# Optimization experiments

Measured on AMD Instinct MI355X. Metric: run time of the kernel, lower is better.

The kernel has to match this reference:

```python
import jax, jax.numpy as jnp
import numpy as np

B, T, C, H = 8, 4096, 768, 64  # batch, seq, input_channels, head size


def setup_inputs() -> dict:
    key = jax.random.key(0)
    k1, k2, k3, k4 = jax.random.split(key, 4)
    scale = 1.0 / np.sqrt(C)
    return {
        "x": jax.random.normal(k1, (B, T, C), dtype=jnp.float32),
        "Wk": jax.random.normal(k2, (C, H), dtype=jnp.float32) * scale,
        "Wq": jax.random.normal(k3, (C, H), dtype=jnp.float32) * scale,
        "Wv": jax.random.normal(k4, (C, H), dtype=jnp.float32) * scale,
    }


def reference(x, Wk, Wq, Wv):
    Bc, Tc, Cc = x.shape
    k = x @ Wk  # [B,T,H]
    q = x @ Wq  # [B,T,H]
    v = x @ Wv  # [B,T,H]
    # Note: original scales by C**-0.5 where C = input_channels
    wei = jnp.einsum("bth,bTh->btT", q, k) * (Cc ** -0.5)
    causal = jnp.tril(jnp.ones((Tc, Tc), dtype=bool))
    wei = jnp.where(causal, wei, -jnp.inf)
    wei = jax.nn.softmax(wei, axis=-1)
    # dropout_prob = 0.0 -> identity
    out = jnp.einsum("btT,bTh->bth", wei, v)
    return out
```

## Files before the change

kernel.cpp:

```cpp
#include <hip/hip_runtime.h>

#define TT 4096
#define CCH 768
#define HH 64
#define BBA 8
#define MROWS (BBA*TT)
#define NCHUNK_PB 288

typedef __attribute__((ext_vector_type(8))) short short8;
typedef __attribute__((ext_vector_type(4))) float floatx4;
#if __has_builtin(__builtin_amdgcn_cvt_pk_bf16_f32)
typedef __attribute__((ext_vector_type(2))) __bf16 bf16x2;
#endif

__device__ inline ushort f2bf(float f) {
    union { float f; unsigned u; } v; v.f = f;
    unsigned r = v.u + 0x7fffu + ((v.u >> 16) & 1u);
    return (ushort)(r >> 16);
}

__device__ inline float bf2f(ushort h) {
    union { unsigned u; float f; } v; v.u = ((unsigned)h) << 16;
    return v.f;
}

__device__ inline unsigned pk_bf16(float a, float b) {
#if __has_builtin(__builtin_amdgcn_cvt_pk_bf16_f32)
    union { bf16x2 v; unsigned u; } cv;
    cv.v = __builtin_amdgcn_cvt_pk_bf16_f32(a, b);
    return cv.u;
#else
    union { float f; unsigned u; } x, y; x.f = a; y.f = b;
    unsigned ra = x.u + 0x7fffu + ((x.u >> 16) & 1u);
    unsigned rb = y.u + 0x7fffu + ((y.u >> 16) & 1u);
    return (ra >> 16) | (rb & 0xffff0000u);
#endif
}

__device__ inline float fast_exp2(float x) {
#if __has_builtin(__builtin_amdgcn_exp2f)
    return __builtin_amdgcn_exp2f(x);
#else
    return exp2f(x);
#endif
}

__global__ __launch_bounds__(256) void wt_kernel(const float* __restrict__ Wq,
                                                 const float* __restrict__ Wk,
                                                 const float* __restrict__ Wv,
                                                 ushort* __restrict__ wt) {
    __shared__ float tile[64][65];
    const int m = blockIdx.x / 12, kt = blockIdx.x % 12;
    const float* W = (m == 0) ? Wq : (m == 1) ? Wk : Wv;
    const int n = threadIdx.x & 63, r0 = threadIdx.x >> 6;
#pragma unroll
    for (int i = 0; i < 16; ++i) {
        int k = r0 * 16 + i;
        tile[k][n] = W[(kt * 64 + k) * 64 + n];
    }
    __syncthreads();
    const int k2 = threadIdx.x & 63, n2 = threadIdx.x >> 6;
#pragma unroll
    for (int i = 0; i < 16; ++i) {
        int nn = n2 * 16 + i;
        wt[(m * 64 + nn) * 768 + kt * 64 + k2] = f2bf(tile[k2][nn]);
    }
}

__global__ __launch_bounds__(256) void proj_kernel(const float* __restrict__ x,
                                                   const ushort* __restrict__ wt,
                                                   ushort* __restrict__ qb,
                                                   ushort* __restrict__ kb,
                                                   ushort* __restrict__ vtg) {
    __shared__ ushort xs[64 * 72];
    __shared__ ushort ws[192 * 72];
    const int tid = threadIdx.x;
    const int w = tid >> 6, lane = tid & 63, c = lane & 15, qd = lane >> 4;
    const int rbase = blockIdx.x * 64;
    const int sr = tid >> 2;
    const int sq = tid & 3;

    floatx4 acc[12];
#pragma unroll
    for (int nt = 0; nt < 12; ++nt) acc[nt] = (floatx4){0.f, 0.f, 0.f, 0.f};

    const float*  xsrc = &x[(size_t)(rbase + sr) * CCH + sq * 16];
    const ushort* wsrc0 = &wt[(size_t)(0 * 64 + sr) * CCH + sq * 16];
    const ushort* wsrc1 = &wt[(size_t)(1 * 64 + sr) * CCH + sq * 16];
    const ushort* wsrc2 = &wt[(size_t)(2 * 64 + sr) * CCH + sq * 16];

    float4 xr[4];
    short8 wr[6];
    xr[0] = *(const float4*)&xsrc[0];  xr[1] = *(const float4*)&xsrc[4];
    xr[2] = *(const float4*)&xsrc[8];  xr[3] = *(const float4*)&xsrc[12];
    wr[0] = *(const short8*)&wsrc0[0]; wr[1] = *(const short8*)&wsrc0[8];
    wr[2] = *(const short8*)&wsrc1[0]; wr[3] = *(const short8*)&wsrc1[8];
    wr[4] = *(const short8*)&wsrc2[0]; wr[5] = *(const short8*)&wsrc2[8];

    for (int kc = 0; kc < CCH; kc += 64) {
        uint4 s0, s1;
        s0.x = pk_bf16(xr[0].x, xr[0].y); s0.y = pk_bf16(xr[0].z, xr[0].w);
        s0.z = pk_bf16(xr[1].x, xr[1].y); s0.w = pk_bf16(xr[1].z, xr[1].w);
        s1.x = pk_bf16(xr[2].x, xr[2].y); s1.y = pk_bf16(xr[2].z, xr[2].w);
        s1.z = pk_bf16(xr[3].x, xr[3].y); s1.w = pk_bf16(xr[3].z, xr[3].w);
        *(uint4*)&xs[sr * 72 + sq * 16]     = s0;
        *(uint4*)&xs[sr * 72 + sq * 16 + 8] = s1;
        *(short8*)&ws[(0 * 64 + sr) * 72 + sq * 16]     = wr[0];
        *(short8*)&ws[(0 * 64 + sr) * 72 + sq * 16 + 8] = wr[1];
        *(short8*)&ws[(1 * 64 + sr) * 72 + sq * 16]     = wr[2];
        *(short8*)&ws[(1 * 64 + sr) * 72 + sq * 16 + 8] = wr[3];
        *(short8*)&ws[(2 * 64 + sr) * 72 + sq * 16]     = wr[4];
        *(short8*)&ws[(2 * 64 + sr) * 72 + sq * 16 + 8] = wr[5];
        __syncthreads();
        if (kc + 64 < CCH) {
            xr[0] = *(const float4*)&xsrc[kc + 64];
            xr[1] = *(const float4*)&xsrc[kc + 68];
            xr[2] = *(const float4*)&xsrc[kc + 72];
            xr[3] = *(const float4*)&xsrc[kc + 76];
            wr[0] = *(const short8*)&wsrc0[kc + 64]; wr[1] = *(const short8*)&wsrc0[kc + 72];
            wr[2] = *(const short8*)&wsrc1[kc + 64]; wr[3] = *(const short8*)&wsrc1[kc + 72];
            wr[4] = *(const short8*)&wsrc2[kc + 64]; wr[5] = *(const short8*)&wsrc2[kc + 72];
        }
        short8 a0 = *(const short8*)&xs[(w * 16 + c) * 72 + qd * 8];
        short8 a1 = *(const short8*)&xs[(w * 16 + c) * 72 + 32 + qd * 8];
#pragma unroll
        for (int nt = 0; nt < 12; ++nt) {
            short8 b0 = *(const short8*)&ws[(nt * 16 + c) * 72 + qd * 8];
            short8 b1 = *(const short8*)&ws[(nt * 16 + c) * 72 + 32 + qd * 8];
            acc[nt] = __builtin_amdgcn_mfma_f32_16x16x32_bf16(a0, b0, acc[nt], 0, 0, 0);
            acc[nt] = __builtin_amdgcn_mfma_f32_16x16x32_bf16(a1, b1, acc[nt], 0, 0, 0);
        }
        __syncthreads();
    }
#pragma unroll
    for (int nt = 0; nt < 8; ++nt) {
        int ncol = nt * 16 + c;
        ushort* dst = (ncol < 64) ? qb : kb;
        int h = ncol & 63;
#pragma unroll
        for (int r = 0; r < 4; ++r) {
            int rg = rbase + w * 16 + qd * 4 + r;
            dst[(size_t)rg * 64 + h] = f2bf(acc[nt][r]);
        }
    }
    const int bb = rbase >> 12;
    const int tbase = (rbase & 4095) + w * 16 + qd * 4;
#pragma unroll
    for (int nt = 8; nt < 12; ++nt) {
        int h = (nt - 8) * 16 + c;
        uint2 val;
        val.x = pk_bf16(acc[nt][0], acc[nt][1]);
        val.y = pk_bf16(acc[nt][2], acc[nt][3]);
        *(uint2*)&vtg[((size_t)(bb * 64 + h)) * 4096 + tbase] = val;
    }
}

__global__ __launch_bounds__(256) void attn_kernel(const ushort* __restrict__ qb,
                                                   const ushort* __restrict__ kb,
                                                   const ushort* __restrict__ vtg,
                                                   float* __restrict__ out,
                                                   ushort* __restrict__ Opart,
                                                   float* __restrict__ Ol,
                                                   int mode) {
    __shared__ ushort Ks[64 * 72];
    __shared__ ushort Vt[64 * 72];
    __shared__ ushort Pl[4][1024];
    const float scale2 = 0.052058773f;
    const int tid = threadIdx.x;
    const int w = tid >> 6, lane = tid & 63, c = lane & 15, qd = lane >> 4;
    const int bx = blockIdx.x;
    const int b = bx & 7, craw = bx >> 3;

    int qt, chunk, nch, cix;
    if (mode == 0) {
        qt = 63 - craw; nch = 1; chunk = 0; cix = qt;
    } else {
        cix = (NCHUNK_PB - 1) - craw;
        int idx, s;
        if      (cix <   8) { idx = 0; s =   0; }
        else if (cix <  24) { idx = 1; s =   8; }
        else if (cix <  48) { idx = 2; s =  24; }
        else if (cix <  80) { idx = 3; s =  48; }
        else if (cix < 120) { idx = 4; s =  80; }
        else if (cix < 168) { idx = 5; s = 120; }
        else if (cix < 224) { idx = 6; s = 168; }
        else                { idx = 7; s = 224; }
        nch = idx + 1;
        int d = cix - s;
        qt = (idx << 3) + d / nch;
        chunk = d - (d / nch) * nch;
    }
    const int n = qt + 1;
    const int kbeg = chunk * n / nch;
    const int kend = (chunk + 1) * n / nch;
    const bool direct = (nch == 1);
    const int qbase = qt * 64;

    const size_t growq = (size_t)(b * TT + qbase + w * 16 + c);
    short8 qf0 = *(const short8*)&qb[growq * 64 + qd * 8];
    short8 qf1 = *(const short8*)&qb[growq * 64 + 32 + qd * 8];
    floatx4 o[4];
#pragma unroll
    for (int nt = 0; nt < 4; ++nt) o[nt] = (floatx4){0.f, 0.f, 0.f, 0.f};
    float lsum = 0.f;

    const int sr = tid >> 2;
    const int sk = (tid & 3) * 16;
    const int vd = tid >> 2;
    const int vk = (tid & 3) * 16;
    const ushort* kbb = &kb[(size_t)(b * TT) * 64];
    const ushort* vbb = &vtg[(size_t)(b * 64) * 4096];

    short8 k0, k1, v0, v1;
    {
        const ushort* srcK = &kbb[((size_t)(kbeg * 64 + sr)) * 64 + sk];
        k0 = *(const short8*)srcK; k1 = *(const short8*)(srcK + 8);
        const ushort* srcV = &vbb[(size_t)vd * 4096 + kbeg * 64 + vk];
        v0 = *(const short8*)srcV; v1 = *(const short8*)(srcV + 8);
    }

    for (int kt = kbeg; kt < kend; ++kt) {
        __syncthreads();
        *(short8*)&Ks[sr * 72 + sk] = k0;
        *(short8*)&Ks[sr * 72 + sk + 8] = k1;
        *(short8*)&Vt[vd * 72 + vk] = v0;
        *(short8*)&Vt[vd * 72 + vk + 8] = v1;
        __syncthreads();
        if (kt + 1 < kend) {
            const ushort* srcK = &kbb[((size_t)((kt + 1) * 64 + sr)) * 64 + sk];
            k0 = *(const short8*)srcK; k1 = *(const short8*)(srcK + 8);
            const ushort* srcV = &vbb[(size_t)vd * 4096 + (kt + 1) * 64 + vk];
            v0 = *(const short8*)srcV; v1 = *(const short8*)(srcV + 8);
        }
        floatx4 st[4];
#pragma unroll
        for (int mt = 0; mt < 4; ++mt) {
            short8 kf0 = *(const short8*)&Ks[(mt * 16 + c) * 72 + qd * 8];
            short8 kf1 = *(const short8*)&Ks[(mt * 16 + c) * 72 + 32 + qd * 8];
            st[mt] = (floatx4){0.f, 0.f, 0.f, 0.f};
            st[mt] = __builtin_amdgcn_mfma_f32_16x16x32_bf16(kf0, qf0, st[mt], 0, 0, 0);
            st[mt] = __builtin_amdgcn_mfma_f32_16x16x32_bf16(kf1, qf1, st[mt], 0, 0, 0);
        }
        float p[16];
#pragma unroll
        for (int mt = 0; mt < 4; ++mt)
#pragma unroll
            for (int r = 0; r < 4; ++r)
                p[mt * 4 + r] = st[mt][r] * scale2;
        if (kt == qt) {
            const int thr = w * 16 + c;
#pragma unroll
            for (int mt = 0; mt < 4; ++mt)
#pragma unroll
                for (int r = 0; r < 4; ++r) {
                    int kl = mt * 16 + qd * 4 + r;
                    if (kl > thr) p[mt * 4 + r] = -1e30f;
                }
        }
#pragma unroll
        for (int i = 0; i < 16; ++i) { p[i] = fast_exp2(p[i]); lsum += p[i]; }
#pragma unroll
        for (int mt = 0; mt < 4; ++mt) {
            uint2 pk;
            pk.x = pk_bf16(p[mt * 4 + 0], p[mt * 4 + 1]);
            pk.y = pk_bf16(p[mt * 4 + 2], p[mt * 4 + 3]);
            int g = 2 * mt + (qd >> 1);
            int off = c * 64 + ((g ^ (c & 7)) << 3) + ((qd & 1) << 2);
            *(uint2*)&Pl[w][off] = pk;
        }
        short8 pf0 = *(const short8*)&Pl[w][c * 64 + (((qd) ^ (c & 7)) << 3)];
        short8 pf1 = *(const short8*)&Pl[w][c * 64 + (((4 + qd) ^ (c & 7)) << 3)];
#pragma unroll
        for (int nt = 0; nt < 4; ++nt) {
            short8 vf0 = *(const short8*)&Vt[(nt * 16 + c) * 72 + qd * 8];
            short8 vf1 = *(const short8*)&Vt[(nt * 16 + c) * 72 + 32 + qd * 8];
            o[nt] = __builtin_amdgcn_mfma_f32_16x16x32_bf16(pf0, vf0, o[nt], 0, 0, 0);
            o[nt] = __builtin_amdgcn_mfma_f32_16x16x32_bf16(pf1, vf1, o[nt], 0, 0, 0);
        }
    }

    float l_run = lsum;
    l_run += __shfl_xor(l_run, 16);
    l_run += __shfl_xor(l_run, 32);

    if (direct) {
#pragma unroll
        for (int r = 0; r < 4; ++r) {
            float lr = __shfl(l_run, qd * 4 + r);
            float inv = 1.f / lr;
            size_t rowg = (size_t)(b * TT) + qbase + w * 16 + qd * 4 + r;
#pragma unroll
            for (int nt = 0; nt < 4; ++nt)
                out[rowg * 64 + nt * 16 + c] = o[nt][r] * inv;
        }
    } else {
        const int slot = b * NCHUNK_PB + cix;
        ushort* Od = Opart + (size_t)slot * 4096;
#pragma unroll
        for (int r = 0; r < 4; ++r) {
            int row = w * 16 + qd * 4 + r;
#pragma unroll
            for (int nt = 0; nt < 4; ++nt)
                Od[row * 64 + nt * 16 + c] = f2bf(o[nt][r]);
        }
        if (qd == 0)
            Ol[(size_t)slot * 64 + w * 16 + c] = l_run;
    }
}

__global__ __launch_bounds__(256) void combine_kernel(const ushort* __restrict__ Opart,
                                                      const float* __restrict__ Ol,
                                                      float* __restrict__ out) {
    const int b = blockIdx.x & 7;
    const int qt = 8 + (blockIdx.x >> 3);
    const int idx = qt >> 3;
    int s;
    if      (idx == 1) s = 8;
    else if (idx == 2) s = 24;
    else if (idx == 3) s = 48;
    else if (idx == 4) s = 80;
    else if (idx == 5) s = 120;
    else if (idx == 6) s = 168;
    else               s = 224;
    const int nch = idx + 1;
    const int c0 = s + (qt - (idx << 3)) * nch;
    const size_t slot0 = (size_t)(b * NCHUNK_PB + c0);
    const int t = threadIdx.x;
    const int col = t & 63, r0 = t >> 6;

    for (int rr = 0; rr < 16; ++rr) {
        int row = (rr << 2) + r0;
        float S = 0.f, A = 0.f;
        for (int i = 0; i < nch; ++i) {
            S += Ol[(slot0 + i) * 64 + row];
            A += bf2f(Opart[(slot0 + i) * 4096 + row * 64 + col]);
        }
        out[((size_t)(b * TT) + qt * 64 + row) * 64 + col] = A / S;
    }
}

extern "C" void kernel_launch(void* const* d_in, const int* in_sizes, int n_in,
                              void* d_out, int out_size, void* d_ws, size_t ws_size,
                              hipStream_t stream) {
    const float* x  = (const float*)d_in[0];
    const float* Wk = (const float*)d_in[1];
    const float* Wq = (const float*)d_in[2];
    const float* Wv = (const float*)d_in[3];
    float* out = (float*)d_out;

    ushort* qbuf = (ushort*)d_ws;
    ushort* kbuf = qbuf + (size_t)MROWS * 64;
    ushort* vbuf = kbuf + (size_t)MROWS * 64;
    ushort* wt   = vbuf + (size_t)MROWS * 64;
    const size_t base = (size_t)MROWS * 64 * 3 * 2 + (size_t)3 * 64 * CCH * 2;
    ushort* Opart = (ushort*)((char*)d_ws + base);
    float*  Ol    = (float*)((char*)d_ws + base + (size_t)BBA * NCHUNK_PB * 4096 * 2);
    const size_t need = base + (size_t)BBA * NCHUNK_PB * 4096 * 2
                             + (size_t)BBA * NCHUNK_PB * 64 * 4;
    const int split = (ws_size >= need) ? 1 : 0;

    wt_kernel<<<36, 256, 0, stream>>>(Wq, Wk, Wv, wt);
    proj_kernel<<<MROWS / 64, 256, 0, stream>>>(x, wt, qbuf, kbuf, vbuf);
    if (split) {
        attn_kernel<<<BBA * NCHUNK_PB, 256, 0, stream>>>(qbuf, kbuf, vbuf, out, Opart, Ol, 1);
        combine_kernel<<<BBA * 56, 256, 0, stream>>>(Opart, Ol, out);
    } else {
        attn_kernel<<<BBA * 64, 256, 0, stream>>>(qbuf, kbuf, vbuf, out, Opart, Ol, 0);
    }
}
```

Measured before the change: 236.4 us.

## Fold softmax scale into Wq and halve projection row tile to 32

The softmax scale (times log2e) is pre-multiplied into Wq when the weights are transposed, which removes one multiply per score in the attention inner loop. The projection kernel now handles 32 rows per block instead of 64 and splits the 12 output column tiles across warps (2 row halves × 2 column halves), doubling the grid and cutting per-thread accumulators from 12 to 6. That should raise occupancy and parallelism, but the weight tile is reloaded twice as often per row of x. Rounding Q to bf16 after scaling also shifts precision slightly.

```diff
diff --git a/kernel.cpp b/kernel.cpp
--- a/kernel.cpp
+++ b/kernel.cpp
@@ -52,11 +52,12 @@
     __shared__ float tile[64][65];
     const int m = blockIdx.x / 12, kt = blockIdx.x % 12;
     const float* W = (m == 0) ? Wq : (m == 1) ? Wk : Wv;
+    const float scl = (m == 0) ? 0.052058773f : 1.0f;
     const int n = threadIdx.x & 63, r0 = threadIdx.x >> 6;
 #pragma unroll
     for (int i = 0; i < 16; ++i) {
         int k = r0 * 16 + i;
-        tile[k][n] = W[(kt * 64 + k) * 64 + n];
+        tile[k][n] = W[(kt * 64 + k) * 64 + n] * scl;
     }
     __syncthreads();
     const int k2 = threadIdx.x & 63, n2 = threadIdx.x >> 6;
@@ -72,86 +73,84 @@
                                                    ushort* __restrict__ qb,
                                                    ushort* __restrict__ kb,
                                                    ushort* __restrict__ vtg) {
-    __shared__ ushort xs[64 * 72];
+    __shared__ ushort xs[32 * 72];
     __shared__ ushort ws[192 * 72];
     const int tid = threadIdx.x;
     const int w = tid >> 6, lane = tid & 63, c = lane & 15, qd = lane >> 4;
-    const int rbase = blockIdx.x * 64;
-    const int sr = tid >> 2;
-    const int sq = tid & 3;
-
-    floatx4 acc[12];
-#pragma unroll
-    for (int nt = 0; nt < 12; ++nt) acc[nt] = (floatx4){0.f, 0.f, 0.f, 0.f};
-
-    const float*  xsrc = &x[(size_t)(rbase + sr) * CCH + sq * 16];
-    const ushort* wsrc0 = &wt[(size_t)(0 * 64 + sr) * CCH + sq * 16];
-    const ushort* wsrc1 = &wt[(size_t)(1 * 64 + sr) * CCH + sq * 16];
-    const ushort* wsrc2 = &wt[(size_t)(2 * 64 + sr) * CCH + sq * 16];
-
-    float4 xr[4];
+    const int rbase = blockIdx.x * 32;
+    const int rowh = (w & 1) * 16;
+    const int nbase = (w >> 1) * 6;
+    const int xr = tid >> 3;
+    const int xc = (tid & 7) * 8;
+    const int swr = tid >> 2;
+    const int swc = (tid & 3) * 16;
+
+    floatx4 acc[6];
+#pragma unroll
+    for (int nt = 0; nt < 6; ++nt) acc[nt] = (floatx4){0.f, 0.f, 0.f, 0.f};
+
+    const float*  xsrc  = &x[(size_t)(rbase + xr) * CCH + xc];
+    const ushort* wsrc0 = &wt[(size_t)(0 * 64 + swr) * CCH + swc];
+    const ushort* wsrc1 = &wt[(size_t)(1 * 64 + swr) * CCH + swc];
+    const ushort* wsrc2 = &wt[(size_t)(2 * 64 + swr) * CCH + swc];
+
+    float4 xr0, xr1;
     short8 wr[6];
-    xr[0] = *(const float4*)&xsrc[0];  xr[1] = *(const float4*)&xsrc[4];
-    xr[2] = *(const float4*)&xsrc[8];  xr[3] = *(const float4*)&xsrc[12];
+    xr0 = *(const float4*)&xsrc[0]; xr1 = *(const float4*)&xsrc[4];
     wr[0] = *(const short8*)&wsrc0[0]; wr[1] = *(const short8*)&wsrc0[8];
     wr[2] = *(const short8*)&wsrc1[0]; wr[3] = *(const short8*)&wsrc1[8];
     wr[4] = *(const short8*)&wsrc2[0]; wr[5] = *(const short8*)&wsrc2[8];
 
     for (int kc = 0; kc < CCH; kc += 64) {
-        uint4 s0, s1;
-        s0.x = pk_bf16(xr[0].x, xr[0].y); s0.y = pk_bf16(xr[0].z, xr[0].w);
-        s0.z = pk_bf16(xr[1].x, xr[1].y); s0.w = pk_bf16(xr[1].z, xr[1].w);
-        s1.x = pk_bf16(xr[2].x, xr[2].y); s1.y = pk_bf16(xr[2].z, xr[2].w);
-        s1.z = pk_bf16(xr[3].x, xr[3].y); s1.w = pk_bf16(xr[3].z, xr[3].w);
-        *(uint4*)&xs[sr * 72 + sq * 16]     = s0;
-        *(uint4*)&xs[sr * 72 + sq * 16 + 8] = s1;
-        *(short8*)&ws[(0 * 64 + sr) * 72 + sq * 16]     = wr[0];
-        *(short8*)&ws[(0 * 64 + sr) * 72 + sq * 16 + 8] = wr[1];
-        *(short8*)&ws[(1 * 64 + sr) * 72 + sq * 16]     = wr[2];
-        *(short8*)&ws[(1 * 64 + sr) * 72 + sq * 16 + 8] = wr[3];
-        *(short8*)&ws[(2 * 64 + sr) * 72 + sq * 16]     = wr[4];
-        *(short8*)&ws[(2 * 64 + sr) * 72 + sq * 16 + 8] = wr[5];
+        uint4 s0;
+        s0.x = pk_bf16(xr0.x, xr0.y); s0.y = pk_bf16(xr0.z, xr0.w);
+        s0.z = pk_bf16(xr1.x, xr1.y); s0.w = pk_bf16(xr1.z, xr1.w);
+        *(uint4*)&xs[xr * 72 + xc] = s0;
+        *(short8*)&ws[(0 * 64 + swr) * 72 + swc]     = wr[0];
+        *(short8*)&ws[(0 * 64 + swr) * 72 + swc + 8] = wr[1];
+        *(short8*)&ws[(1 * 64 + swr) * 72 + swc]     = wr[2];
+        *(short8*)&ws[(1 * 64 + swr) * 72 + swc + 8] = wr[3];
+        *(short8*)&ws[(2 * 64 + swr) * 72 + swc]     = wr[4];
+        *(short8*)&ws[(2 * 64 + swr) * 72 + swc + 8] = wr[5];
         __syncthreads();
         if (kc + 64 < CCH) {
-            xr[0] = *(const float4*)&xsrc[kc + 64];
-            xr[1] = *(const float4*)&xsrc[kc + 68];
-            xr[2] = *(const float4*)&xsrc[kc + 72];
-            xr[3] = *(const float4*)&xsrc[kc + 76];
+            xr0 = *(const float4*)&xsrc[kc + 64];
+            xr1 = *(const float4*)&xsrc[kc + 68];
             wr[0] = *(const short8*)&wsrc0[kc + 64]; wr[1] = *(const short8*)&wsrc0[kc + 72];
             wr[2] = *(const short8*)&wsrc1[kc + 64]; wr[3] = *(const short8*)&wsrc1[kc + 72];
             wr[4] = *(const short8*)&wsrc2[kc + 64]; wr[5] = *(const short8*)&wsrc2[kc + 72];
         }
-        short8 a0 = *(const short8*)&xs[(w * 16 + c) * 72 + qd * 8];
-        short8 a1 = *(const short8*)&xs[(w * 16 + c) * 72 + 32 + qd * 8];
-#pragma unroll
-        for (int nt = 0; nt < 12; ++nt) {
-            short8 b0 = *(const short8*)&ws[(nt * 16 + c) * 72 + qd * 8];
-            short8 b1 = *(const short8*)&ws[(nt * 16 + c) * 72 + 32 + qd * 8];
+        short8 a0 = *(const short8*)&xs[(rowh + c) * 72 + qd * 8];
+        short8 a1 = *(const short8*)&xs[(rowh + c) * 72 + 32 + qd * 8];
+#pragma unroll
+        for (int nt = 0; nt < 6; ++nt) {
+            short8 b0 = *(const short8*)&ws[((nbase + nt) * 16 + c) * 72 + qd * 8];
+            short8 b1 = *(const short8*)&ws[((nbase + nt) * 16 + c) * 72 + 32 + qd * 8];
             acc[nt] = __builtin_amdgcn_mfma_f32_16x16x32_bf16(a0, b0, acc[nt], 0, 0, 0);
             acc[nt] = __builtin_amdgcn_mfma_f32_16x16x32_bf16(a1, b1, acc[nt], 0, 0, 0);
         }
         __syncthreads();
     }
-#pragma unroll
-    for (int nt = 0; nt < 8; ++nt) {
-        int ncol = nt * 16 + c;
-        ushort* dst = (ncol < 64) ? qb : kb;
-        int h = ncol & 63;
-#pragma unroll
-        for (int r = 0; r < 4; ++r) {
-            int rg = rbase + w * 16 + qd * 4 + r;
-            dst[(size_t)rg * 64 + h] = f2bf(acc[nt][r]);
-        }
-    }
     const int bb = rbase >> 12;
-    const int tbase = (rbase & 4095) + w * 16 + qd * 4;
-#pragma unroll
-    for (int nt = 8; nt < 12; ++nt) {
-        int h = (nt - 8) * 16 + c;
-        uint2 val;
-        val.x = pk_bf16(acc[nt][0], acc[nt][1]);
-        val.y = pk_bf16(acc[nt][2], acc[nt][3]);
-        *(uint2*)&vtg[((size_t)(bb * 64 + h)) * 4096 + tbase] = val;
+#pragma unroll
+    for (int nt = 0; nt < 6; ++nt) {
+        int ncol = (nbase + nt) * 16 + c;
+        if (ncol < 128) {
+            ushort* dst = (ncol < 64) ? qb : kb;
+            int h = ncol & 63;
+#pragma unroll
+            for (int r = 0; r < 4; ++r) {
+                int rg = rbase + rowh + qd * 4 + r;
+                dst[(size_t)rg * 64 + h] = f2bf(acc[nt][r]);
+            }
+        } else {
+            int h = ncol - 128;
+            int trow = (rbase & 4095) + rowh + qd * 4;
+            uint2 val;
+            val.x = pk_bf16(acc[nt][0], acc[nt][1]);
+            val.y = pk_bf16(acc[nt][2], acc[nt][3]);
+            *(uint2*)&vtg[((size_t)(bb * 64 + h)) * 4096 + trow] = val;
+        }
     }
 }
 
@@ -165,7 +164,6 @@
     __shared__ ushort Ks[64 * 72];
     __shared__ ushort Vt[64 * 72];
     __shared__ ushort Pl[4][1024];
-    const float scale2 = 0.052058773f;
     const int tid = threadIdx.x;
     const int w = tid >> 6, lane = tid & 63, c = lane & 15, qd = lane >> 4;
     const int bx = blockIdx.x;
@@ -246,7 +244,7 @@
         for (int mt = 0; mt < 4; ++mt)
 #pragma unroll
             for (int r = 0; r < 4; ++r)
-                p[mt * 4 + r] = st[mt][r] * scale2;
+                p[mt * 4 + r] = st[mt][r];
         if (kt == qt) {
             const int thr = w * 16 + c;
 #pragma unroll
@@ -360,7 +358,7 @@
     const int split = (ws_size >= need) ? 1 : 0;
 
     wt_kernel<<<36, 256, 0, stream>>>(Wq, Wk, Wv, wt);
-    proj_kernel<<<MROWS / 64, 256, 0, stream>>>(x, wt, qbuf, kbuf, vbuf);
+    proj_kernel<<<MROWS / 32, 256, 0, stream>>>(x, wt, qbuf, kbuf, vbuf);
     if (split) {
         attn_kernel<<<BBA * NCHUNK_PB, 256, 0, stream>>>(qbuf, kbuf, vbuf, out, Opart, Ol, 1);
         combine_kernel<<<BBA * 56, 256, 0, stream>>>(Opart, Ol, out);
```

Result: slower. 242.0 us (+2.4%).

## Double query rows per attention block and fold softmax scale into Wq

Applied to the files above, without the earlier changes.

Each attention block now processes 128 query rows (two 16-row sub-tiles per wave) instead of 64. Every K/V tile loaded into shared memory therefore feeds twice as many MFMAs, which cuts global and LDS traffic per unit of work and halves the number of split-K chunks and partial outputs. The softmax scale is folded into Wq during weight conversion, which removes the per-score multiply. The fallback path for a too-small workspace is dropped, so the split path always runs. The costs are higher register and LDS use per block, fewer blocks in flight, and bf16 rounding of the pre-scaled Q.

```diff
diff --git a/kernel.cpp b/kernel.cpp
--- a/kernel.cpp
+++ b/kernel.cpp
@@ -5,7 +5,7 @@
 #define HH 64
 #define BBA 8
 #define MROWS (BBA*TT)
-#define NCHUNK_PB 288
+#define NCHUNK2 144
 
 typedef __attribute__((ext_vector_type(8))) short short8;
 typedef __attribute__((ext_vector_type(4))) float floatx4;
@@ -52,11 +52,12 @@
     __shared__ float tile[64][65];
     const int m = blockIdx.x / 12, kt = blockIdx.x % 12;
     const float* W = (m == 0) ? Wq : (m == 1) ? Wk : Wv;
+    const float scl = (m == 0) ? 0.052058773f : 1.0f;
     const int n = threadIdx.x & 63, r0 = threadIdx.x >> 6;
 #pragma unroll
     for (int i = 0; i < 16; ++i) {
         int k = r0 * 16 + i;
-        tile[k][n] = W[(kt * 64 + k) * 64 + n];
+        tile[k][n] = W[(kt * 64 + k) * 64 + n] * scl;
     }
     __syncthreads();
     const int k2 = threadIdx.x & 63, n2 = threadIdx.x >> 6;
@@ -160,54 +161,45 @@
                                                    const ushort* __restrict__ vtg,
                                                    float* __restrict__ out,
                                                    ushort* __restrict__ Opart,
-                                                   float* __restrict__ Ol,
-                                                   int mode) {
+                                                   float* __restrict__ Ol) {
     __shared__ ushort Ks[64 * 72];
     __shared__ ushort Vt[64 * 72];
-    __shared__ ushort Pl[4][1024];
-    const float scale2 = 0.052058773f;
+    __shared__ ushort Pl[4][2048];
     const int tid = threadIdx.x;
     const int w = tid >> 6, lane = tid & 63, c = lane & 15, qd = lane >> 4;
     const int bx = blockIdx.x;
     const int b = bx & 7, craw = bx >> 3;
 
-    int qt, chunk, nch, cix;
-    if (mode == 0) {
-        qt = 63 - craw; nch = 1; chunk = 0; cix = qt;
-    } else {
-        cix = (NCHUNK_PB - 1) - craw;
-        int idx, s;
-        if      (cix <   8) { idx = 0; s =   0; }
-        else if (cix <  24) { idx = 1; s =   8; }
-        else if (cix <  48) { idx = 2; s =  24; }
-        else if (cix <  80) { idx = 3; s =  48; }
-        else if (cix < 120) { idx = 4; s =  80; }
-        else if (cix < 168) { idx = 5; s = 120; }
-        else if (cix < 224) { idx = 6; s = 168; }
-        else                { idx = 7; s = 224; }
-        nch = idx + 1;
-        int d = cix - s;
-        qt = (idx << 3) + d / nch;
-        chunk = d - (d / nch) * nch;
-    }
-    const int n = qt + 1;
+    const int cix = (NCHUNK2 - 1) - craw;
+    int g = 0;
+#pragma unroll
+    for (int t = 1; t < 8; ++t) if (cix >= 2 * t * (t + 1)) g = t;
+    const int nch = g + 1;
+    const int d = cix - 2 * g * (g + 1);
+    const int qt = 4 * g + d / nch;
+    const int chunk = d - (d / nch) * nch;
+    const int n = 2 * qt + 2;
     const int kbeg = chunk * n / nch;
     const int kend = (chunk + 1) * n / nch;
     const bool direct = (nch == 1);
-    const int qbase = qt * 64;
-
-    const size_t growq = (size_t)(b * TT + qbase + w * 16 + c);
-    short8 qf0 = *(const short8*)&qb[growq * 64 + qd * 8];
-    short8 qf1 = *(const short8*)&qb[growq * 64 + 32 + qd * 8];
-    floatx4 o[4];
-#pragma unroll
-    for (int nt = 0; nt < 4; ++nt) o[nt] = (floatx4){0.f, 0.f, 0.f, 0.f};
-    float lsum = 0.f;
+    const int qbase = qt * 128;
+
+    short8 qf[2][2];
+#pragma unroll
+    for (int sub = 0; sub < 2; ++sub) {
+        const size_t gq = (size_t)(b * TT + qbase + w * 32 + sub * 16 + c);
+        qf[sub][0] = *(const short8*)&qb[gq * 64 + qd * 8];
+        qf[sub][1] = *(const short8*)&qb[gq * 64 + 32 + qd * 8];
+    }
+    floatx4 o[2][4];
+#pragma unroll
+    for (int sub = 0; sub < 2; ++sub)
+#pragma unroll
+        for (int nt = 0; nt < 4; ++nt) o[sub][nt] = (floatx4){0.f, 0.f, 0.f, 0.f};
+    float lsum[2] = {0.f, 0.f};
 
     const int sr = tid >> 2;
     const int sk = (tid & 3) * 16;
-    const int vd = tid >> 2;
-    const int vk = (tid & 3) * 16;
     const ushort* kbb = &kb[(size_t)(b * TT) * 64];
     const ushort* vbb = &vtg[(size_t)(b * 64) * 4096];
 
@@ -215,7 +207,7 @@
     {
         const ushort* srcK = &kbb[((size_t)(kbeg * 64 + sr)) * 64 + sk];
         k0 = *(const short8*)srcK; k1 = *(const short8*)(srcK + 8);
-        const ushort* srcV = &vbb[(size_t)vd * 4096 + kbeg * 64 + vk];
+        const ushort* srcV = &vbb[(size_t)sr * 4096 + kbeg * 64 + sk];
         v0 = *(const short8*)srcV; v1 = *(const short8*)(srcV + 8);
     }
 
@@ -223,88 +215,103 @@
         __syncthreads();
         *(short8*)&Ks[sr * 72 + sk] = k0;
         *(short8*)&Ks[sr * 72 + sk + 8] = k1;
-        *(short8*)&Vt[vd * 72 + vk] = v0;
-        *(short8*)&Vt[vd * 72 + vk + 8] = v1;
+        *(short8*)&Vt[sr * 72 + sk] = v0;
+        *(short8*)&Vt[sr * 72 + sk + 8] = v1;
         __syncthreads();
         if (kt + 1 < kend) {
             const ushort* srcK = &kbb[((size_t)((kt + 1) * 64 + sr)) * 64 + sk];
             k0 = *(const short8*)srcK; k1 = *(const short8*)(srcK + 8);
-            const ushort* srcV = &vbb[(size_t)vd * 4096 + (kt + 1) * 64 + vk];
+            const ushort* srcV = &vbb[(size_t)sr * 4096 + (kt + 1) * 64 + sk];
             v0 = *(const short8*)srcV; v1 = *(const short8*)(srcV + 8);
         }
-        floatx4 st[4];
+        floatx4 st[2][4];
 #pragma unroll
         for (int mt = 0; mt < 4; ++mt) {
             short8 kf0 = *(const short8*)&Ks[(mt * 16 + c) * 72 + qd * 8];
             short8 kf1 = *(const short8*)&Ks[(mt * 16 + c) * 72 + 32 + qd * 8];
-            st[mt] = (floatx4){0.f, 0.f, 0.f, 0.f};
-            st[mt] = __builtin_amdgcn_mfma_f32_16x16x32_bf16(kf0, qf0, st[mt], 0, 0, 0);
-            st[mt] = __builtin_amdgcn_mfma_f32_16x16x32_bf16(kf1, qf1, st[mt], 0, 0, 0);
-        }
-        float p[16];
-#pragma unroll
-        for (int mt = 0; mt < 4; ++mt)
-#pragma unroll
-            for (int r = 0; r < 4; ++r)
-                p[mt * 4 + r] = st[mt][r] * scale2;
-        if (kt == qt) {
-            const int thr = w * 16 + c;
-#pragma unroll
-            for (int mt = 0; mt < 4; ++mt)
+            st[0][mt] = (floatx4){0.f, 0.f, 0.f, 0.f};
+            st[0][mt] = __builtin_amdgcn_mfma_f32_16x16x32_bf16(kf0, qf[0][0], st[0][mt], 0, 0, 0);
+            st[0][mt] = __builtin_amdgcn_mfma_f32_16x16x32_bf16(kf1, qf[0][1], st[0][mt], 0, 0, 0);
+            st[1][mt] = (floatx4){0.f, 0.f, 0.f, 0.f};
+            st[1][mt] = __builtin_amdgcn_mfma_f32_16x16x32_bf16(kf0, qf[1][0], st[1][mt], 0, 0, 0);
+            st[1][mt] = __builtin_amdgcn_mfma_f32_16x16x32_bf16(kf1, qf[1][1], st[1][mt], 0, 0, 0);
+        }
+        const bool domask = (kt >= 2 * qt);
+#pragma unroll
+        for (int sub = 0; sub < 2; ++sub) {
+            const int thr = qbase + w * 32 + sub * 16 + c;
+            float ls = 0.f;
+#pragma unroll
+            for (int mt = 0; mt < 4; ++mt) {
+                float e[4];
 #pragma unroll
                 for (int r = 0; r < 4; ++r) {
-                    int kl = mt * 16 + qd * 4 + r;
-                    if (kl > thr) p[mt * 4 + r] = -1e30f;
+                    float v = st[sub][mt][r];
+                    if (domask) {
+                        int kl = kt * 64 + mt * 16 + qd * 4 + r;
+                        if (kl > thr) v = -1e30f;
+                    }
+                    e[r] = fast_exp2(v);
+                    ls += e[r];
                 }
-        }
-#pragma unroll
-        for (int i = 0; i < 16; ++i) { p[i] = fast_exp2(p[i]); lsum += p[i]; }
-#pragma unroll
-        for (int mt = 0; mt < 4; ++mt) {
-            uint2 pk;
-            pk.x = pk_bf16(p[mt * 4 + 0], p[mt * 4 + 1]);
-            pk.y = pk_bf16(p[mt * 4 + 2], p[mt * 4 + 3]);
-            int g = 2 * mt + (qd >> 1);
-            int off = c * 64 + ((g ^ (c & 7)) << 3) + ((qd & 1) << 2);
-            *(uint2*)&Pl[w][off] = pk;
-        }
-        short8 pf0 = *(const short8*)&Pl[w][c * 64 + (((qd) ^ (c & 7)) << 3)];
-        short8 pf1 = *(const short8*)&Pl[w][c * 64 + (((4 + qd) ^ (c & 7)) << 3)];
+                uint2 pk;
+                pk.x = pk_bf16(e[0], e[1]);
+                pk.y = pk_bf16(e[2], e[3]);
+                int gg = 2 * mt + (qd >> 1);
+                int off = sub * 1024 + c * 64 + ((gg ^ (c & 7)) << 3) + ((qd & 1) << 2);
+                *(uint2*)&Pl[w][off] = pk;
+            }
+            lsum[sub] += ls;
+        }
+        short8 pf00 = *(const short8*)&Pl[w][c * 64 + (((qd) ^ (c & 7)) << 3)];
+        short8 pf01 = *(const short8*)&Pl[w][c * 64 + (((4 + qd) ^ (c & 7)) << 3)];
+        short8 pf10 = *(const short8*)&Pl[w][1024 + c * 64 + (((qd) ^ (c & 7)) << 3)];
+        short8 pf11 = *(const short8*)&Pl[w][1024 + c * 64 + (((4 + qd) ^ (c & 7)) << 3)];
 #pragma unroll
         for (int nt = 0; nt < 4; ++nt) {
             short8 vf0 = *(const short8*)&Vt[(nt * 16 + c) * 72 + qd * 8];
             short8 vf1 = *(const short8*)&Vt[(nt * 16 + c) * 72 + 32 + qd * 8];
-            o[nt] = __builtin_amdgcn_mfma_f32_16x16x32_bf16(pf0, vf0, o[nt], 0, 0, 0);
-            o[nt] = __builtin_amdgcn_mfma_f32_16x16x32_bf16(pf1, vf1, o[nt], 0, 0, 0);
-        }
-    }
-
-    float l_run = lsum;
-    l_run += __shfl_xor(l_run, 16);
-    l_run += __shfl_xor(l_run, 32);
+            o[0][nt] = __builtin_amdgcn_mfma_f32_16x16x32_bf16(pf00, vf0, o[0][nt], 0, 0, 0);
+            o[0][nt] = __builtin_amdgcn_mfma_f32_16x16x32_bf16(pf01, vf1, o[0][nt], 0, 0, 0);
+            o[1][nt] = __builtin_amdgcn_mfma_f32_16x16x32_bf16(pf10, vf0, o[1][nt], 0, 0, 0);
+            o[1][nt] = __builtin_amdgcn_mfma_f32_16x16x32_bf16(pf11, vf1, o[1][nt], 0, 0, 0);
+        }
+    }
+
+#pragma unroll
+    for (int sub = 0; sub < 2; ++sub) {
+        lsum[sub] += __shfl_xor(lsum[sub], 16);
+        lsum[sub] += __shfl_xor(lsum[sub], 32);
+    }
 
     if (direct) {
 #pragma unroll
-        for (int r = 0; r < 4; ++r) {
-            float lr = __shfl(l_run, qd * 4 + r);
-            float inv = 1.f / lr;
-            size_t rowg = (size_t)(b * TT) + qbase + w * 16 + qd * 4 + r;
-#pragma unroll
-            for (int nt = 0; nt < 4; ++nt)
-                out[rowg * 64 + nt * 16 + c] = o[nt][r] * inv;
-        }
+        for (int sub = 0; sub < 2; ++sub)
+#pragma unroll
+            for (int r = 0; r < 4; ++r) {
+                float lr = __shfl(lsum[sub], qd * 4 + r);
+                float inv = 1.f / lr;
+                size_t rowg = (size_t)(b * TT) + qbase + w * 32 + sub * 16 + qd * 4 + r;
+#pragma unroll
+                for (int nt = 0; nt < 4; ++nt)
+                    out[rowg * 64 + nt * 16 + c] = o[sub][nt][r] * inv;
+            }
     } else {
-        const int slot = b * NCHUNK_PB + cix;
-        ushort* Od = Opart + (size_t)slot * 4096;
-#pragma unroll
-        for (int r = 0; r < 4; ++r) {
-            int row = w * 16 + qd * 4 + r;
-#pragma unroll
-            for (int nt = 0; nt < 4; ++nt)
-                Od[row * 64 + nt * 16 + c] = f2bf(o[nt][r]);
-        }
-        if (qd == 0)
-            Ol[(size_t)slot * 64 + w * 16 + c] = l_run;
+        const int slot = b * NCHUNK2 + cix;
+        ushort* Od = Opart + (size_t)slot * 8192;
+#pragma unroll
+        for (int sub = 0; sub < 2; ++sub)
+#pragma unroll
+            for (int r = 0; r < 4; ++r) {
+                int row = w * 32 + sub * 16 + qd * 4 + r;
+#pragma unroll
+                for (int nt = 0; nt < 4; ++nt)
+                    Od[row * 64 + nt * 16 + c] = f2bf(o[sub][nt][r]);
+            }
+        if (qd == 0) {
+            Ol[(size_t)slot * 128 + w * 32 + c] = lsum[0];
+            Ol[(size_t)slot * 128 + w * 32 + 16 + c] = lsum[1];
+        }
     }
 }
 
@@ -312,30 +319,22 @@
                                                       const float* __restrict__ Ol,
                                                       float* __restrict__ out) {
     const int b = blockIdx.x & 7;
-    const int qt = 8 + (blockIdx.x >> 3);
-    const int idx = qt >> 3;
-    int s;
-    if      (idx == 1) s = 8;
-    else if (idx == 2) s = 24;
-    else if (idx == 3) s = 48;
-    else if (idx == 4) s = 80;
-    else if (idx == 5) s = 120;
-    else if (idx == 6) s = 168;
-    else               s = 224;
-    const int nch = idx + 1;
-    const int c0 = s + (qt - (idx << 3)) * nch;
-    const size_t slot0 = (size_t)(b * NCHUNK_PB + c0);
+    const int qq = 4 + (blockIdx.x >> 3);
+    const int g = qq >> 2;
+    const int nch = g + 1;
+    const int c0 = 2 * g * (g + 1) + (qq - 4 * g) * nch;
+    const size_t slot0 = (size_t)(b * NCHUNK2 + c0);
     const int t = threadIdx.x;
     const int col = t & 63, r0 = t >> 6;
 
-    for (int rr = 0; rr < 16; ++rr) {
+    for (int rr = 0; rr < 32; ++rr) {
         int row = (rr << 2) + r0;
         float S = 0.f, A = 0.f;
         for (int i = 0; i < nch; ++i) {
-            S += Ol[(slot0 + i) * 64 + row];
-            A += bf2f(Opart[(slot0 + i) * 4096 + row * 64 + col]);
-        }
-        out[((size_t)(b * TT) + qt * 64 + row) * 64 + col] = A / S;
+            S += Ol[(slot0 + i) * 128 + row];
+            A += bf2f(Opart[(slot0 + i) * 8192 + row * 64 + col]);
+        }
+        out[((size_t)(b * TT) + qq * 128 + row) * 64 + col] = A / S;
     }
 }
 
@@ -354,17 +353,10 @@
     ushort* wt   = vbuf + (size_t)MROWS * 64;
     const size_t base = (size_t)MROWS * 64 * 3 * 2 + (size_t)3 * 64 * CCH * 2;
     ushort* Opart = (ushort*)((char*)d_ws + base);
-    float*  Ol    = (float*)((char*)d_ws + base + (size_t)BBA * NCHUNK_PB * 4096 * 2);
-    const size_t need = base + (size_t)BBA * NCHUNK_PB * 4096 * 2
-                             + (size_t)BBA * NCHUNK_PB * 64 * 4;
-    const int split = (ws_size >= need) ? 1 : 0;
+    float*  Ol    = (float*)((char*)d_ws + base + (size_t)BBA * NCHUNK2 * 8192 * 2);
 
     wt_kernel<<<36, 256, 0, stream>>>(Wq, Wk, Wv, wt);
     proj_kernel<<<MROWS / 64, 256, 0, stream>>>(x, wt, qbuf, kbuf, vbuf);
-    if (split) {
-        attn_kernel<<<BBA * NCHUNK_PB, 256, 0, stream>>>(qbuf, kbuf, vbuf, out, Opart, Ol, 1);
-        combine_kernel<<<BBA * 56, 256, 0, stream>>>(Opart, Ol, out);
-    } else {
-        attn_kernel<<<BBA * 64, 256, 0, stream>>>(qbuf, kbuf, vbuf, out, Opart, Ol, 0);
-    }
-}
+    attn_kernel<<<BBA * NCHUNK2, 256, 0, stream>>>(qbuf, kbuf, vbuf, out, Opart, Ol);
+    combine_kernel<<<BBA * 28, 256, 0, stream>>>(Opart, Ol, out);
+}
```

Result: slower. 269.3 us (+13.9%).
